# Performance work log

Measured on AMD Instinct MI355X. Metric: run time of the kernel, lower is better.

The kernel has to match this reference:

```python
import jax, jax.numpy as jnp
import numpy as np

B, T, N, D = 32, 12, 325, 64
H = 4           # geo_num_heads == t_num_heads
HD = D // H     # head_dim = 16
M_SP = 32       # spatial frequency modes (min(32, N//2))
M_T = T // 2    # temporal frequency modes (all low modes)
SCALE = HD ** -0.5


def _lin(x, W):
    # torch nn.Linear (no bias): y = x @ W.T, W: [out, in]
    return jnp.einsum('btnd,ed->btne', x, W)


def _spatial(x, Wq, Wk, Wv, weights_Q, sp_modes):
    # FEDformer-style frequency attention over the node axis N
    q, k, v = _lin(x, Wq), _lin(x, Wk), _lin(x, Wv)          # [B,T,N,D]
    prep = lambda y: y.reshape(B, T, N, H, HD).transpose(0, 1, 3, 4, 2)  # [B,T,H,HD,N]
    qn = prep(q) / jnp.linalg.norm(q)   # global Frobenius norm (torch.norm with no dim)
    kn = prep(k) / jnp.linalg.norm(k)
    vn = prep(v)
    # rfft over nodes, gather selected modes (scatter-into-zeros in torch == gather here
    # since target indices are 0..M-1)
    qf = jnp.fft.rfft(qn, axis=-1)[..., sp_modes]            # [B,T,H,HD,M] c64
    kf = jnp.fft.rfft(kn, axis=-1)[..., sp_modes]
    vf = jnp.fft.rfft(vn, axis=-1)[..., sp_modes]
    M = M_SP
    qg = qf.transpose(0, 1, 2, 4, 3)[:, :, :, :, None, :]    # [B,T,H,M,1,HD]
    wq = jnp.broadcast_to(weights_Q.astype(jnp.complex64), (B, T, H, M, M - 1, HD))
    q_cat = jnp.concatenate([qg, wq], axis=4)                # [B,T,H,M,M,HD]
    kg = kf.transpose(0, 1, 2, 4, 3)[:, :, :, None, :, :]    # [B,T,H,1,M,HD]
    att = kg * jnp.conj(q_cat) * SCALE                       # [B,T,H,M,M,HD] c64
    att = jax.nn.softmax(jnp.abs(att), axis=-2).astype(jnp.complex64)
    att = att.transpose(0, 1, 2, 3, 5, 4)                    # [B,T,H,M,HD,M]
    vg = vf[:, :, :, None, :, :]                             # [B,T,H,1,HD,M]
    out = (vg * jnp.conj(att)).mean(axis=3)                  # [B,T,H,HD,M]
    out_ft = jnp.zeros((B, T, H, HD, N // 2 + 1), jnp.complex64).at[..., sp_modes].set(out)
    y = jnp.fft.irfft(out_ft, n=N, axis=-1)                  # [B,T,H,HD,N]
    return y.transpose(0, 1, 4, 2, 3).reshape(B, T, N, D)


def _temporal(x, Wq, Wk, Wv, weights_Q_t, t_modes):
    # frequency attention over the time axis T with causal (tril) mask.
    # NOTE: torch reshapes the [B,T,N,D] buffer directly as [B,N,T,H,HD] (raw view),
    # so we replicate that exact buffer reinterpretation.
    q, k, v = _lin(x, Wq), _lin(x, Wk), _lin(x, Wv)
    prep = lambda y: y.reshape(B, N, T, H, HD).transpose(0, 1, 3, 4, 2)  # [B,N,H,HD,T]
    qn = prep(q); kn = prep(k); vn = prep(v)
    qn = qn / jnp.linalg.norm(qn)
    kn = kn / jnp.linalg.norm(kn)
    qf = jnp.fft.rfft(qn, axis=-1)[..., t_modes]             # [B,N,H,HD,Mt]
    kf = jnp.fft.rfft(kn, axis=-1)[..., t_modes]
    vf = jnp.fft.rfft(vn, axis=-1)[..., t_modes]
    Mt = M_T
    qg = qf.transpose(0, 1, 2, 4, 3)[:, :, :, :, None, :]    # [B,N,H,Mt,1,HD]
    wq = jnp.broadcast_to(weights_Q_t.astype(jnp.complex64), (B, N, H, Mt, Mt - 1, HD))
    q_cat = jnp.concatenate([qg, wq], axis=4)                # [B,N,H,Mt,Mt,HD]
    kg = kf.transpose(0, 1, 2, 4, 3)[:, :, :, :, None, :]    # [B,N,H,Mt,1,HD] (unsqueeze(4) in torch)
    att = kg * jnp.conj(q_cat) * SCALE                       # [B,N,H,Mt,Mt,HD]
    att = att.transpose(0, 1, 2, 5, 3, 4)                    # [B,N,H,HD,Mt,Mt]
    mask = jnp.tril(jnp.ones((Mt, Mt), jnp.float32))
    att = att * mask                                         # zero above diagonal
    attw = jax.nn.softmax(jnp.abs(att), axis=-1).astype(jnp.complex64)
    vg = vf[..., None]                                       # [B,N,H,HD,Mt,1]
    out = (vg * jnp.conj(attw)).mean(axis=-1)                # [B,N,H,HD,Mt]
    out_ft = jnp.zeros((B, N, H, HD, T // 2 + 1), jnp.complex64).at[..., t_modes].set(out)
    y = jnp.fft.irfft(out_ft, n=T, axis=-1)                  # [B,N,H,HD,T]
    return y.transpose(0, 4, 1, 2, 3).reshape(B, T, N, D)


def _gcn(x, adj, W_fc1, W_mlp, b_mlp):
    a = adj / jnp.sum(adj, axis=1, keepdims=True)            # row-normalized
    agg = jnp.einsum('btkd,nk->btnd', x, a)
    h = jnp.einsum('btnd,ed->btne', agg, W_fc1)              # fc1 (no bias)
    return jnp.einsum('btnd,ed->btne', h, W_mlp) + b_mlp     # mlp (bias)


def _forward(x, adj, Wq_geo, Wk_geo, Wv_geo, Wq_t, Wk_t, Wv_t,
             W_fc1, W_mlp, b_mlp, weights_Q, weights_Q_t, sp_modes, t_modes):
    gcn_out = _gcn(x, adj, W_fc1, W_mlp, b_mlp)
    sp_x = _spatial(x, Wq_geo, Wk_geo, Wv_geo, weights_Q, sp_modes)
    te_x = _temporal(x, Wq_t, Wk_t, Wv_t, weights_Q_t, t_modes)
    return gcn_out + sp_x + te_x   # proj_drop is identity (p=0)


def setup_inputs() -> dict:
    key = jax.random.key(0)
    ks = jax.random.split(key, 13)
    w = lambda k, s: jax.random.normal(k, s, dtype=jnp.float32) * 0.05
    rng = np.random.default_rng(0)
    sp_modes = np.sort(rng.permutation(N // 2)[:M_SP]).astype(np.int32)
    t_modes = np.arange(M_T, dtype=np.int32)  # modes_T == T//2 selects all low modes
    return {
        'x': jax.random.normal(ks[0], (B, T, N, D), dtype=jnp.float32),
        'adj': jax.random.uniform(ks[1], (N, N), dtype=jnp.float32),
        'Wq_geo': w(ks[2], (D, D)), 'Wk_geo': w(ks[3], (D, D)), 'Wv_geo': w(ks[4], (D, D)),
        'Wq_t': w(ks[5], (D, D)), 'Wk_t': w(ks[6], (D, D)), 'Wv_t': w(ks[7], (D, D)),
        'W_fc1': w(ks[8], (D, D)), 'W_mlp': w(ks[9], (D, D)), 'b_mlp': w(ks[10], (D,)),
        'weights_Q': jax.random.normal(ks[11], (M_SP, M_SP - 1, HD), dtype=jnp.float32),
        'weights_Q_t': jax.random.normal(ks[12], (M_T, M_T - 1, HD), dtype=jnp.float32),
        'sp_modes': jnp.asarray(sp_modes),
        't_modes': jnp.asarray(t_modes),
    }


def reference(x, adj, Wq_geo, Wk_geo, Wv_geo, Wq_t, Wk_t, Wv_t,
              W_fc1, W_mlp, b_mlp, weights_Q, weights_Q_t, sp_modes, t_modes):
    return _forward(x, adj, Wq_geo, Wk_geo, Wv_geo, Wq_t, Wk_t, Wv_t,
                    W_fc1, W_mlp, b_mlp, weights_Q, weights_Q_t, sp_modes, t_modes)
```

## Files before the change

kernel.cpp:

```cpp
#include <hip/hip_runtime.h>


typedef unsigned short u16;
typedef short short8 __attribute__((ext_vector_type(8)));
typedef float floatx4 __attribute__((ext_vector_type(4)));

__device__ __forceinline__ u16 f2bf(float f) {
  union { float fp; unsigned int u; } v; v.fp = f;
  unsigned int x = v.u;
  x += 0x7FFF + ((x >> 16) & 1);
  return (u16)(x >> 16);
}

constexpr size_t OFF_NORM = 4096;
constexpr size_t OFF_WQA  = 8208;
constexpr size_t OFF_ANB  = 24080;
constexpr size_t OFF_TB   = 81280;
constexpr size_t OFF_T2   = 102080;
constexpr size_t OFF_XCT  = 898912;
constexpr size_t OFF_WBB  = 5224288;
constexpr size_t OFF_WSPB = 5230432;
constexpr size_t OFF_WVTB = 5236576;
constexpr size_t OFF_SQQ  = 5240000;
constexpr size_t OFF_SQK  = 6026432;
constexpr size_t OFF_VFR  = 6812864;
constexpr size_t OFF_VFI  = 7599296;
constexpr size_t OFF_XA   = 13211488;

__global__ __launch_bounds__(256) void k_prep(const float* __restrict__ Wmlp,
                                              const float* __restrict__ Wfc1,
                                              const float* __restrict__ wQ,
                                              const float* __restrict__ Wq,
                                              const float* __restrict__ Wk,
                                              const float* __restrict__ Wv,
                                              const int* __restrict__ sp_modes,
                                              float* __restrict__ ws) {
  const int tid = threadIdx.x;
  const int blk = blockIdx.x;
  u16* WBBu = (u16*)(ws + OFF_WBB);
  if (blk == 0) {
    for (int i = tid; i < 512; i += 256) ws[OFF_NORM + i] = 0.f;
    for (int o = tid; o < 4096; o += 256) {
      int g = o >> 6, dd = o & 63;
      float s = 0.f;
      for (int e = 0; e < 64; ++e)
        s = fmaf(Wmlp[g * 64 + e], Wfc1[e * 64 + dd], s);
      WBBu[o] = f2bf(s);
    }
  } else if (blk < 9) {
    for (int i = (blk - 1) * 256 + tid; i < 15872; i += 2048)
      ws[OFF_WQA + i] = fabsf(wQ[i]);
  } else if (blk < 21) {
    const int j = blk - 9;
    u16* T2B = (u16*)(ws + OFF_T2);
    u16* TB = (u16*)(ws + OFF_TB);
    for (int jj = j; jj < 32; jj += 12) {
      const int f = sp_modes[jj];
      const float wgt = (f == 0) ? 1.f : 2.f;
      const int row_re = 8 * (jj >> 2) + (jj & 3);
      const int row_im = row_re + 4;
      for (int n = tid; n < 352; n += 256) {
        float c = 0.f, s = 0.f;
        if (n < 325) {
          int mm = (f * n) % 325;
          float th = 6.283185307179586f * (float)mm * (1.f / 325.f);
          c = cosf(th);
          s = sinf(th);
        }
        TB[(size_t)row_re * 352 + n] = f2bf(c);
        TB[(size_t)row_im * 352 + n] = f2bf(-s);
        if (n < 325) {
          T2B[(size_t)n * 64 + 2 * jj] = f2bf(wgt * (1.f / 325.f) * c);
          T2B[(size_t)n * 64 + 2 * jj + 1] = f2bf(-wgt * (1.f / 325.f) * s);
        }
      }
    }
  } else if (blk == 21) {
    u16* WSPBu = (u16*)(ws + OFF_WSPB);
    for (int i = tid; i < 12288; i += 256) {
      const int r = i >> 6, e = i & 63;
      const float* src = (r < 64) ? Wq : (r < 128) ? Wk : Wv;
      WSPBu[i] = f2bf(src[(size_t)(r & 63) * 64 + e]);
    }
  } else {
    for (int i = tid; i < 8192; i += 256) {
      const int r = i >> 6, e = i & 63;
      const float* src = (r < 64) ? Wq : Wk;
      WBBu[4096 + i] = f2bf(src[(size_t)(r & 63) * 64 + e]);
    }
  }
}

__global__ __launch_bounds__(256) void k_mega(const float* __restrict__ x,
                                              const float* __restrict__ adj,
                                              const float* __restrict__ Wvt,
                                              float* __restrict__ ws) {
  __shared__ __align__(16) float smem[11520];
  const int tid = threadIdx.x;
  const int blk = blockIdx.x;
  const int lane = tid & 63, wv = tid >> 6;
  const int lc = lane & 15, quad = lane >> 4;

  if (blk < 384) {
    const int bt = blk;
    u16* XBu = (u16*)smem;

    const u16* TB = (const u16*)(ws + OFF_TB);
    const u16* WSPBu = (const u16*)(ws + OFF_WSPB);
    const float* xb = x + (size_t)bt * 20800;
    const int br = tid & 31, be0 = (tid >> 5) * 8;

    {
      float va[4][8];
#pragma unroll
      for (int g = 0; g < 3; ++g) {
        const int nkc = (g < 2) ? 4 : 3;
#pragma unroll
        for (int u = 0; u < 4; ++u) {
          if (u >= nkc) break;
          const int k0 = (g * 4 + u) * 32;
          if (k0 + br < 325) {
            const float* src = xb + (size_t)(k0 + br) * 64 + be0;
            *(float4*)&va[u][0] = *(const float4*)src;
            *(float4*)&va[u][4] = *(const float4*)(src + 4);
          } else {
#pragma unroll
            for (int w = 0; w < 8; ++w) va[u][w] = 0.f;
          }
        }
#pragma unroll
        for (int u = 0; u < 4; ++u) {
          if (u >= nkc) break;
          const int k0 = (g * 4 + u) * 32;
#pragma unroll
          for (int w = 0; w < 8; ++w)
            XBu[(be0 + w) * 360 + k0 + br] = f2bf(va[u][w]);
        }
      }
    }
    __syncthreads();

    floatx4 accA[4] = {};
#pragma unroll
    for (int kc = 0; kc < 11; ++kc) {
      const short8 af = *(const short8*)&TB[(size_t)(16 * wv + lc) * 352 + kc * 32 + quad * 8];
#pragma unroll
      for (int t = 0; t < 4; ++t) {
        const short8 bf_ = *(const short8*)&XBu[(t * 16 + lc) * 360 + kc * 32 + quad * 8];
        accA[t] = __builtin_amdgcn_mfma_f32_16x16x32_bf16(af, bf_, accA[t], 0, 0, 0);
      }
    }
    __syncthreads();

    u16* xfl2 = XBu;
#pragma unroll
    for (int t = 0; t < 4; ++t)
#pragma unroll
      for (int r = 0; r < 4; ++r)
        xfl2[(t >> 1) * 2560 + (16 * wv + quad * 4 + r) * 40 + (t & 1) * 16 + lc] =
            f2bf(accA[t][r]);
    __syncthreads();

    floatx4 acc2[12] = {};
#pragma unroll
    for (int kc2 = 0; kc2 < 2; ++kc2) {
      const short8 af2 = *(const short8*)&xfl2[kc2 * 2560 + (16 * wv + lc) * 40 + quad * 8];
#pragma unroll
      for (int t = 0; t < 12; ++t) {
        const short8 bf2 = *(const short8*)&WSPBu[(t * 16 + lc) * 64 + kc2 * 32 + quad * 8];
        acc2[t] = __builtin_amdgcn_mfma_f32_16x16x32_bf16(af2, bf2, acc2[t], 0, 0, 0);
      }
    }

    float* g_sqq = ws + OFF_SQQ + (size_t)bt * 2048;
    float* g_sqk = ws + OFF_SQK + (size_t)bt * 2048;
    float* g_vfr = ws + OFF_VFR + (size_t)bt * 2048;
    float* g_vfi = ws + OFF_VFI + (size_t)bt * 2048;
    {
      const int fb = 8 * wv + ((quad >= 2) ? 4 : 0);
      const int isim = quad & 1;
#pragma unroll
      for (int t = 0; t < 12; ++t) {
        const int mat = t >> 2;
        const int d = (t & 3) * 16 + lc;
#pragma unroll
        for (int r = 0; r < 4; ++r) {
          const float v = acc2[t][r];
          if (mat == 2) {
            if (isim) g_vfi[(fb + r) * 64 + d] = v;
            else g_vfr[(fb + r) * 64 + d] = v;
          } else {
            const float s2 = v * v + __shfl_xor(v * v, 16);
            if (!isim) {
              if (mat == 0) g_sqq[(fb + r) * 64 + d] = sqrtf(s2);
              else g_sqk[(fb + r) * 64 + d] = sqrtf(s2);
            }
          }
        }
      }
    }
  } else if (blk < 1359) {
    const int blk2 = blk - 384;
    u16* XAu = (u16*)smem;
    float* red = smem + 4608;
    const size_t base = (size_t)blk2 * 128;
    const u16* WBBu = (const u16*)(ws + OFF_WBB);

    for (int i = tid; i < 2048; i += 256) {
      const int row = i >> 4, e0 = (i & 15) * 4;
      const float4 v = *(const float4*)(x + (base + row) * 64 + e0);
      u16* dst = &XAu[row * 72 + e0];
      dst[0] = f2bf(v.x); dst[1] = f2bf(v.y); dst[2] = f2bf(v.z); dst[3] = f2bf(v.w);
    }
    __syncthreads();

    short8 afc[2][2];
#pragma unroll
    for (int kc = 0; kc < 2; ++kc)
#pragma unroll
      for (int mi = 0; mi < 2; ++mi)
        afc[mi][kc] = *(const short8*)&XAu[(32 * wv + 16 * mi + lc) * 72 + kc * 32 + quad * 8];

    floatx4 acc[2][4] = {};
#pragma unroll
    for (int kc = 0; kc < 2; ++kc)
#pragma unroll
      for (int ni = 0; ni < 4; ++ni) {
        const short8 bf_ = *(const short8*)&WBBu[(ni * 16 + lc) * 64 + kc * 32 + quad * 8];
#pragma unroll
        for (int mi = 0; mi < 2; ++mi)
          acc[mi][ni] = __builtin_amdgcn_mfma_f32_16x16x32_bf16(afc[mi][kc], bf_, acc[mi][ni], 0, 0, 0);
      }

    float sq = 0.f, sk = 0.f;
#pragma unroll
    for (int ni = 0; ni < 8; ++ni) {
      floatx4 a0 = {}, a1 = {};
#pragma unroll
      for (int kc = 0; kc < 2; ++kc) {
        const short8 bf_ = *(const short8*)&WBBu[
            (size_t)(64 + (ni >> 2) * 64 + (ni & 3) * 16 + lc) * 64 + kc * 32 + quad * 8];
        a0 = __builtin_amdgcn_mfma_f32_16x16x32_bf16(afc[0][kc], bf_, a0, 0, 0, 0);
        a1 = __builtin_amdgcn_mfma_f32_16x16x32_bf16(afc[1][kc], bf_, a1, 0, 0, 0);
      }
      float s = 0.f;
#pragma unroll
      for (int reg = 0; reg < 4; ++reg)
        s = fmaf(a0[reg], a0[reg], fmaf(a1[reg], a1[reg], s));
      if (ni < 4) sq += s; else sk += s;
    }
    for (int off = 32; off > 0; off >>= 1) {
      sq += __shfl_down(sq, off);
      sk += __shfl_down(sk, off);
    }
    if (lane == 0) { red[wv] = sq; red[8 + wv] = sk; }
    __syncthreads();

    u16* xcT = XAu;
#pragma unroll
    for (int ni = 0; ni < 4; ++ni)
#pragma unroll
      for (int mi = 0; mi < 2; ++mi)
#pragma unroll
        for (int reg = 0; reg < 4; ++reg)
          xcT[(ni * 16 + lc) * 132 + 32 * wv + 16 * mi + quad * 4 + reg] =
              f2bf(acc[mi][ni][reg]);
    __syncthreads();
    u16* XCT = (u16*)(ws + OFF_XCT);
    for (int i = tid; i < 8192; i += 256) {
      const int d = i >> 7, r = i & 127;
      const unsigned int row = (unsigned int)(base + r);
      const unsigned int bt = row / 325u;
      const unsigned int n = row - bt * 325u;
      XCT[(size_t)bt * 22528 + (size_t)d * 352 + n] = xcT[d * 132 + r];
    }
    if (tid == 0)
      atomicAdd(&ws[OFF_NORM + 32 * (size_t)(blk2 & 15) + 0],
                red[0] + red[1] + red[2] + red[3]);
    if (tid == 1)
      atomicAdd(&ws[OFF_NORM + 32 * (size_t)(blk2 & 15) + 1],
                red[8] + red[9] + red[10] + red[11]);
  } else if (blk < 2009) {
    const int idx = (blk - 1359) * 256 + tid;
    if (idx >= 32 * 325 * 16) return;
    const int dq = idx & 15;
    const int n = (idx >> 4) % 325;
    const int b = idx / (16 * 325);
    const float* xp = x + ((size_t)b * 3900 + (size_t)n * 12) * 64 + dq * 4;
    float4 s = make_float4(0.f, 0.f, 0.f, 0.f);
    float sign = 1.f;
    for (int k = 0; k < 12; ++k) {
      const float4 v = *(const float4*)(xp + (size_t)k * 64);
      s.x += sign * v.x; s.y += sign * v.y; s.z += sign * v.z; s.w += sign * v.w;
      sign = -sign;
    }
    *(float4*)(ws + OFF_XA + ((size_t)b * 325 + n) * 64 + dq * 4) = s;
  } else if (blk < 2334) {
    const int n = blk - 2009;
    float* red = smem;
    float p = 0.f;
    for (int k = tid; k < 325; k += 256) p += adj[n * 325 + k];
    red[tid] = p;
    __syncthreads();
    for (int s2 = 128; s2 > 0; s2 >>= 1) {
      if (tid < s2) red[tid] += red[tid + s2];
      __syncthreads();
    }
    const float inv = 1.f / red[0];
    u16* ANB = (u16*)(ws + OFF_ANB);
    for (int k = tid; k < 352; k += 256)
      ANB[(size_t)n * 352 + k] = (k < 325) ? f2bf(adj[n * 325 + k] * inv) : (u16)0;
  } else if (blk < 2430) {
    const int idx = (blk - 2334) * 256 + tid;
    u16* p = (u16*)(ws + OFF_XCT) + (size_t)(idx >> 6) * 22528 + (size_t)(idx & 63) * 352;
    for (int c = 325; c < 352; ++c) p[c] = 0;
  } else {
    u16* WVTBu = (u16*)(ws + OFF_WVTB);
    for (int i = tid; i < 4096; i += 256) WVTBu[i] = f2bf(Wvt[i]);
  }
}

__global__ __launch_bounds__(256) void k_final3(const float* __restrict__ x,
                                                const float* __restrict__ bmlp,
                                                float* __restrict__ ws,
                                                float* __restrict__ out) {
  __shared__ __align__(16) float smem[8448];
  float* asq = smem;
  float* askl = smem + 2048;
  float* wbar = smem + 4096;
  unsigned int* oftu = (unsigned int*)(smem + 6144);
  const u16* oft16 = (const u16*)oftu;

  const int tid = threadIdx.x;
  const int bt = blockIdx.x / 3, mc = blockIdx.x % 3;
  const int m0 = mc * 128;
  const int wave = tid >> 6, lane = tid & 63;
  const int quad = lane >> 4, lc = lane & 15;

  float nq = 0.f, nk = 0.f;
#pragma unroll
  for (int k2 = 0; k2 < 16; ++k2) {
    const float2 v = *(const float2*)(ws + OFF_NORM + 32 * (size_t)k2);
    nq += v.x; nk += v.y;
  }
  const float inv_nq = rsqrtf(nq);
  const float inv_nk = rsqrtf(nk);

  for (int i = tid; i < 2048; i += 256) {
    asq[i] = ws[OFF_SQQ + (size_t)bt * 2048 + i];
    askl[i] = 0.25f * inv_nk * ws[OFF_SQK + (size_t)bt * 2048 + i];
    wbar[i] = 0.f;
  }
  __syncthreads();
  {
    const int d = tid & 63, fb2 = tid >> 6, hd = d & 15;
    const float* wqa = ws + OFF_WQA;
    float wacc[32];
#pragma unroll
    for (int j = 0; j < 32; ++j) wacc[j] = 0.f;
    for (int r8 = 0; r8 < 8; ++r8) {
      const int m = fb2 + (r8 << 2);
      const float aq = inv_nq * asq[m * 64 + d];
      float sv[32];
      float mx = -1e30f;
#pragma unroll
      for (int j = 0; j < 32; ++j) {
        const float a = (j == 0) ? aq : wqa[(m * 31 + (j - 1)) * 16 + hd];
        const float s = askl[j * 64 + d] * a;
        sv[j] = s;
        mx = fmaxf(mx, s);
      }
      float sum = 0.f;
#pragma unroll
      for (int j = 0; j < 32; ++j) {
        const float ev = __expf(sv[j] - mx);
        sv[j] = ev;
        sum += ev;
      }
      const float sc = 0.03125f / sum;
#pragma unroll
      for (int j = 0; j < 32; ++j) wacc[j] += sv[j] * sc;
    }
#pragma unroll
    for (int j = 0; j < 32; ++j) atomicAdd(&wbar[j * 64 + d], wacc[j]);
  }
  __syncthreads();
  for (int i2 = tid; i2 < 2048; i2 += 256) {
    const int j = i2 >> 6, d = i2 & 63;
    const float w = wbar[j * 64 + d];
    const unsigned int lo = f2bf(ws[OFF_VFR + (size_t)bt * 2048 + j * 64 + d] * w);
    const unsigned int hi = f2bf(ws[OFF_VFI + (size_t)bt * 2048 + j * 64 + d] * w);
    oftu[d * 36 + j] = lo | (hi << 16);
  }
  __syncthreads();

  const u16* ANB = (const u16*)(ws + OFF_ANB);
  const u16* T2B = (const u16*)(ws + OFF_T2);
  const u16* XCT = (const u16*)(ws + OFF_XCT) + (size_t)bt * 22528;
  const u16* WVTBu = (const u16*)(ws + OFF_WVTB);

  const int b = bt / 12, t = bt - b * 12;
  const float sgn12 = ((t & 1) ? -1.f : 1.f) * (1.f / 12.f);

  floatx4 acc[2][4] = {};

#pragma unroll
  for (int c13 = 0; c13 < 13; ++c13) {
    const bool gcn = (c13 < 11);
    const int acol = gcn ? c13 * 32 : (c13 - 11) * 32;
    short8 af[2], bf_[4];
#pragma unroll
    for (int mi = 0; mi < 2; ++mi) {
      const int gr = m0 + wave * 32 + mi * 16 + lc;
      short8 a = {};
      if (gr < 325)
        a = gcn ? *(const short8*)&ANB[(size_t)gr * 352 + acol + quad * 8]
                : *(const short8*)&T2B[(size_t)gr * 64 + acol + quad * 8];
      af[mi] = a;
    }
#pragma unroll
    for (int ni = 0; ni < 4; ++ni)
      bf_[ni] = gcn ? *(const short8*)&XCT[(size_t)(ni * 16 + lc) * 352 + acol + quad * 8]
                    : *(const short8*)&oft16[(ni * 16 + lc) * 72 + acol + quad * 8];
#pragma unroll
    for (int mi = 0; mi < 2; ++mi)
#pragma unroll
      for (int ni = 0; ni < 4; ++ni)
        acc[mi][ni] = __builtin_amdgcn_mfma_f32_16x16x32_bf16(
            af[mi], bf_[ni], acc[mi][ni], 0, 0, 0);
  }

#pragma unroll
  for (int kc = 0; kc < 2; ++kc) {
    const int k0 = kc * 32 + quad * 8;
    short8 af[2];
#pragma unroll
    for (int mi = 0; mi < 2; ++mi) {
      const int nr = m0 + wave * 32 + mi * 16 + lc;
      short8 a = {};
      if (nr < 325) {
        const float* xp = x + ((size_t)b * 3900 + (size_t)nr * 12 + t) * 64 + k0;
        const float* xap = ws + OFF_XA + ((size_t)b * 325 + nr) * 64 + k0;
        float xv[8], av[8];
        *(float4*)xv = *(const float4*)xp;
        *(float4*)(xv + 4) = *(const float4*)(xp + 4);
        *(float4*)av = *(const float4*)xap;
        *(float4*)(av + 4) = *(const float4*)(xap + 4);
#pragma unroll
        for (int u = 0; u < 8; ++u)
          a[u] = (short)f2bf((xv[u] - sgn12 * av[u]) * (1.f / 6.f));
      }
      af[mi] = a;
    }
#pragma unroll
    for (int ni = 0; ni < 4; ++ni) {
      const short8 bf_ = *(const short8*)&WVTBu[(size_t)(ni * 16 + lc) * 64 + k0];
#pragma unroll
      for (int mi = 0; mi < 2; ++mi)
        acc[mi][ni] = __builtin_amdgcn_mfma_f32_16x16x32_bf16(
            af[mi], bf_, acc[mi][ni], 0, 0, 0);
    }
  }

#pragma unroll
  for (int ni = 0; ni < 4; ++ni) {
    const int d = ni * 16 + lc;
    const float bias = bmlp[d];
#pragma unroll
    for (int mi = 0; mi < 2; ++mi) {
#pragma unroll
      for (int reg = 0; reg < 4; ++reg) {
        const int n = m0 + wave * 32 + mi * 16 + quad * 4 + reg;
        if (n >= 325) continue;
        out[((size_t)bt * 325 + n) * 64 + d] = acc[mi][ni][reg] + bias;
      }
    }
  }
}

extern "C" void kernel_launch(void* const* d_in, const int* in_sizes, int n_in,
                              void* d_out, int out_size, void* d_ws, size_t ws_size,
                              hipStream_t stream) {
  const float* x = (const float*)d_in[0];
  const float* adj = (const float*)d_in[1];
  const float* Wq_g = (const float*)d_in[2];
  const float* Wk_g = (const float*)d_in[3];
  const float* Wv_g = (const float*)d_in[4];
  const float* Wv_t = (const float*)d_in[7];
  const float* Wfc1 = (const float*)d_in[8];
  const float* Wmlp = (const float*)d_in[9];
  const float* bmlp = (const float*)d_in[10];
  const float* wQ = (const float*)d_in[11];
  const int* sp_modes = (const int*)d_in[13];
  float* ws = (float*)d_ws;
  float* out = (float*)d_out;

  (void)in_sizes; (void)n_in; (void)out_size; (void)ws_size;

  k_prep<<<23, 256, 0, stream>>>(Wmlp, Wfc1, wQ, Wq_g, Wk_g, Wv_g, sp_modes, ws);
  k_mega<<<2431, 256, 0, stream>>>(x, adj, Wv_t, ws);
  k_final3<<<1152, 256, 0, stream>>>(x, bmlp, ws, out);
}
```

Measured before the change: 281.1 us.

## Hoist per-bt spectral softmax into separate kernel, swizzle final block order

```diff
diff --git a/kernel.cpp b/kernel.cpp
--- a/kernel.cpp
+++ b/kernel.cpp
@@ -17,6 +17,7 @@
 constexpr size_t OFF_ANB  = 24080;
 constexpr size_t OFF_TB   = 81280;
 constexpr size_t OFF_T2   = 102080;
+constexpr size_t OFF_OFT  = 112480;
 constexpr size_t OFF_XCT  = 898912;
 constexpr size_t OFF_WBB  = 5224288;
 constexpr size_t OFF_WSPB = 5230432;
@@ -92,8 +93,6 @@
 }
 
 __global__ __launch_bounds__(256) void k_mega(const float* __restrict__ x,
-                                              const float* __restrict__ adj,
-                                              const float* __restrict__ Wvt,
                                               float* __restrict__ ws) {
   __shared__ __align__(16) float smem[11520];
   const int tid = threadIdx.x;
@@ -280,7 +279,7 @@
     if (tid == 1)
       atomicAdd(&ws[OFF_NORM + 32 * (size_t)(blk2 & 15) + 1],
                 red[8] + red[9] + red[10] + red[11]);
-  } else if (blk < 2009) {
+  } else {
     const int idx = (blk - 1359) * 256 + tid;
     if (idx >= 32 * 325 * 16) return;
     const int dq = idx & 15;
@@ -295,8 +294,84 @@
       sign = -sign;
     }
     *(float4*)(ws + OFF_XA + ((size_t)b * 325 + n) * 64 + dq * 4) = s;
-  } else if (blk < 2334) {
-    const int n = blk - 2009;
+  }
+}
+
+__global__ __launch_bounds__(256) void k_phasec(const float* __restrict__ adj,
+                                                const float* __restrict__ Wvt,
+                                                float* __restrict__ ws) {
+  __shared__ __align__(16) float smem[10240];
+  const int tid = threadIdx.x;
+  const int blk = blockIdx.x;
+
+  if (blk < 384) {
+    const int bt = blk;
+    float* asq = smem;
+    float* askl = smem + 2048;
+    float* vfre = smem + 4096;
+    float* vfim = smem + 6144;
+    float* wbar = smem + 8192;
+
+    float g_nq = 0.f, g_nk = 0.f;
+#pragma unroll
+    for (int k2 = 0; k2 < 16; ++k2) {
+      const float2 v = *(const float2*)(ws + OFF_NORM + 32 * (size_t)k2);
+      g_nq += v.x; g_nk += v.y;
+    }
+    const float inv_nq = rsqrtf(g_nq);
+    const float inv_nk = rsqrtf(g_nk);
+
+    for (int i = tid; i < 2048; i += 256) {
+      asq[i] = ws[OFF_SQQ + (size_t)bt * 2048 + i];
+      askl[i] = 0.25f * inv_nk * ws[OFF_SQK + (size_t)bt * 2048 + i];
+      vfre[i] = ws[OFF_VFR + (size_t)bt * 2048 + i];
+      vfim[i] = ws[OFF_VFI + (size_t)bt * 2048 + i];
+      wbar[i] = 0.f;
+    }
+    __syncthreads();
+    {
+      const int d = tid & 63, fb2 = tid >> 6, hd = d & 15;
+      const float* wqa = ws + OFF_WQA;
+      float wacc[32];
+#pragma unroll
+      for (int j = 0; j < 32; ++j) wacc[j] = 0.f;
+      for (int r8 = 0; r8 < 8; ++r8) {
+        const int m = fb2 + (r8 << 2);
+        const float aq = inv_nq * asq[m * 64 + d];
+        float sv[32];
+        float mx = -1e30f;
+#pragma unroll
+        for (int j = 0; j < 32; ++j) {
+          const float a = (j == 0) ? aq : wqa[(m * 31 + (j - 1)) * 16 + hd];
+          const float s = askl[j * 64 + d] * a;
+          sv[j] = s;
+          mx = fmaxf(mx, s);
+        }
+        float sum = 0.f;
+#pragma unroll
+        for (int j = 0; j < 32; ++j) {
+          const float ev = __expf(sv[j] - mx);
+          sv[j] = ev;
+          sum += ev;
+        }
+        const float sc = 0.03125f / sum;
+#pragma unroll
+        for (int j = 0; j < 32; ++j) wacc[j] += sv[j] * sc;
+      }
+#pragma unroll
+      for (int j = 0; j < 32; ++j) atomicAdd(&wbar[j * 64 + d], wacc[j]);
+    }
+    __syncthreads();
+    unsigned int* OFTu = (unsigned int*)(ws + OFF_OFT) + (size_t)bt * 2048;
+    for (int i2 = tid; i2 < 2048; i2 += 256) {
+      const int d = i2 >> 5, j = i2 & 31;
+      const float w = wbar[j * 64 + d];
+      const unsigned int lo = f2bf(vfre[j * 64 + d] * w);
+      const unsigned int hi = f2bf(vfim[j * 64 + d] * w);
+      OFTu[i2] = lo | (hi << 16);
+    }
+  } else if (blk < 709) {
+    const int n = blk - 384;
     float* red = smem;
     float p = 0.f;
     for (int k = tid; k < 325; k += 256) p += adj[n * 325 + k];
@@ -310,8 +385,8 @@
     u16* ANB = (u16*)(ws + OFF_ANB);
     for (int k = tid; k < 352; k += 256)
       ANB[(size_t)n * 352 + k] = (k < 325) ? f2bf(adj[n * 325 + k] * inv) : (u16)0;
-  } else if (blk < 2430) {
-    const int idx = (blk - 2334) * 256 + tid;
+  } else if (blk < 805) {
+    const int idx = (blk - 709) * 256 + tid;
     u16* p = (u16*)(ws + OFF_XCT) + (size_t)(idx >> 6) * 22528 + (size_t)(idx & 63) * 352;
     for (int c = 325; c < 352; ++c) p[c] = 0;
   } else {
@@ -320,83 +395,21 @@
   }
 }
 
-__global__ __launch_bounds__(256) void k_final3(const float* __restrict__ x,
+__global__ __launch_bounds__(256) void k_final2(const float* __restrict__ x,
                                                 const float* __restrict__ bmlp,
                                                 float* __restrict__ ws,
                                                 float* __restrict__ out) {
-  __shared__ __align__(16) float smem[8448];
-  float* asq = smem;
-  float* askl = smem + 2048;
-  float* wbar = smem + 4096;
-  unsigned int* oftu = (unsigned int*)(smem + 6144);
-  const u16* oft16 = (const u16*)oftu;
-
   const int tid = threadIdx.x;
-  const int bt = blockIdx.x / 3, mc = blockIdx.x % 3;
+  const int wg = (blockIdx.x & 7) * 144 + (blockIdx.x >> 3);
+  const int bt = wg / 3, mc = wg % 3;
   const int m0 = mc * 128;
   const int wave = tid >> 6, lane = tid & 63;
   const int quad = lane >> 4, lc = lane & 15;
 
-  float nq = 0.f, nk = 0.f;
-#pragma unroll
-  for (int k2 = 0; k2 < 16; ++k2) {
-    const float2 v = *(const float2*)(ws + OFF_NORM + 32 * (size_t)k2);
-    nq += v.x; nk += v.y;
-  }
-  const float inv_nq = rsqrtf(nq);
-  const float inv_nk = rsqrtf(nk);
-
-  for (int i = tid; i < 2048; i += 256) {
-    asq[i] = ws[OFF_SQQ + (size_t)bt * 2048 + i];
-    askl[i] = 0.25f * inv_nk * ws[OFF_SQK + (size_t)bt * 2048 + i];
-    wbar[i] = 0.f;
-  }
-  __syncthreads();
-  {
-    const int d = tid & 63, fb2 = tid >> 6, hd = d & 15;
-    const float* wqa = ws + OFF_WQA;
-    float wacc[32];
-#pragma unroll
-    for (int j = 0; j < 32; ++j) wacc[j] = 0.f;
-    for (int r8 = 0; r8 < 8; ++r8) {
-      const int m = fb2 + (r8 << 2);
-      const float aq = inv_nq * asq[m * 64 + d];
-      float sv[32];
-      float mx = -1e30f;
-#pragma unroll
-      for (int j = 0; j < 32; ++j) {
-        const float a = (j == 0) ? aq : wqa[(m * 31 + (j - 1)) * 16 + hd];
-        const float s = askl[j * 64 + d] * a;
-        sv[j] = s;
-        mx = fmaxf(mx, s);
-      }
-      float sum = 0.f;
-#pragma unroll
-      for (int j = 0; j < 32; ++j) {
-        const float ev = __expf(sv[j] - mx);
-        sv[j] = ev;
-        sum += ev;
-      }
-      const float sc = 0.03125f / sum;
-#pragma unroll
-      for (int j = 0; j < 32; ++j) wacc[j] += sv[j] * sc;
-    }
-#pragma unroll
-    for (int j = 0; j < 32; ++j) atomicAdd(&wbar[j * 64 + d], wacc[j]);
-  }
-  __syncthreads();
-  for (int i2 = tid; i2 < 2048; i2 += 256) {
-    const int j = i2 >> 6, d = i2 & 63;
-    const float w = wbar[j * 64 + d];
-    const unsigned int lo = f2bf(ws[OFF_VFR + (size_t)bt * 2048 + j * 64 + d] * w);
-    const unsigned int hi = f2bf(ws[OFF_VFI + (size_t)bt * 2048 + j * 64 + d] * w);
-    oftu[d * 36 + j] = lo | (hi << 16);
-  }
-  __syncthreads();
-
   const u16* ANB = (const u16*)(ws + OFF_ANB);
   const u16* T2B = (const u16*)(ws + OFF_T2);
   const u16* XCT = (const u16*)(ws + OFF_XCT) + (size_t)bt * 22528;
+  const u16* OFT = (const u16*)(ws + OFF_OFT) + (size_t)bt * 4096;
   const u16* WVTBu = (const u16*)(ws + OFF_WVTB);
 
   const int b = bt / 12, t = bt - b * 12;
@@ -407,21 +420,23 @@
 #pragma unroll
   for (int c13 = 0; c13 < 13; ++c13) {
     const bool gcn = (c13 < 11);
+    const u16* Asrc = gcn ? ANB : T2B;
+    const int astr = gcn ? 352 : 64;
     const int acol = gcn ? c13 * 32 : (c13 - 11) * 32;
+    const u16* Bsrc = gcn ? XCT : OFT;
+    const int bstr = gcn ? 352 : 64;
     short8 af[2], bf_[4];
 #pragma unroll
     for (int mi = 0; mi < 2; ++mi) {
       const int gr = m0 + wave * 32 + mi * 16 + lc;
       short8 a = {};
       if (gr < 325)
-        a = gcn ? *(const short8*)&ANB[(size_t)gr * 352 + acol + quad * 8]
-                : *(const short8*)&T2B[(size_t)gr * 64 + acol + quad * 8];
+        a = *(const short8*)&Asrc[(size_t)gr * astr + acol + quad * 8];
       af[mi] = a;
     }
 #pragma unroll
     for (int ni = 0; ni < 4; ++ni)
-      bf_[ni] = gcn ? *(const short8*)&XCT[(size_t)(ni * 16 + lc) * 352 + acol + quad * 8]
-                    : *(const short8*)&oft16[(ni * 16 + lc) * 72 + acol + quad * 8];
+      bf_[ni] = *(const short8*)&Bsrc[(size_t)(ni * 16 + lc) * bstr + acol + quad * 8];
 #pragma unroll
     for (int mi = 0; mi < 2; ++mi)
 #pragma unroll
@@ -498,6 +513,7 @@
   (void)in_sizes; (void)n_in; (void)out_size; (void)ws_size;
 
   k_prep<<<23, 256, 0, stream>>>(Wmlp, Wfc1, wQ, Wq_g, Wk_g, Wv_g, sp_modes, ws);
-  k_mega<<<2431, 256, 0, stream>>>(x, adj, Wv_t, ws);
-  k_final3<<<1152, 256, 0, stream>>>(x, bmlp, ws, out);
+  k_mega<<<2009, 256, 0, stream>>>(x, ws);
+  k_phasec<<<806, 256, 0, stream>>>(adj, Wv_t, ws);
+  k_final2<<<1152, 256, 0, stream>>>(x, bmlp, ws, out);
 }
```

New measurement: 237.1 us. 15.6% less time.

## Process all node chunks per block to avoid recomputing spectral softmax weights

Applied to the files above, without the earlier changes.

```diff
diff --git a/kernel.cpp b/kernel.cpp
--- a/kernel.cpp
+++ b/kernel.cpp
@@ -320,35 +320,38 @@
   }
 }
 
-__global__ __launch_bounds__(256) void k_final3(const float* __restrict__ x,
+__global__ __launch_bounds__(256) void k_final4(const float* __restrict__ x,
                                                 const float* __restrict__ bmlp,
                                                 float* __restrict__ ws,
                                                 float* __restrict__ out) {
-  __shared__ __align__(16) float smem[8448];
+  __shared__ __align__(16) float smem[10240];
   float* asq = smem;
   float* askl = smem + 2048;
-  float* wbar = smem + 4096;
-  unsigned int* oftu = (unsigned int*)(smem + 6144);
+  float* vfre = smem + 4096;
+  float* vfim = smem + 6144;
+  float* wbar = smem + 8192;
+  unsigned int* oftu = (unsigned int*)smem;
   const u16* oft16 = (const u16*)oftu;
 
   const int tid = threadIdx.x;
-  const int bt = blockIdx.x / 3, mc = blockIdx.x % 3;
-  const int m0 = mc * 128;
+  const int bt = blockIdx.x;
   const int wave = tid >> 6, lane = tid & 63;
   const int quad = lane >> 4, lc = lane & 15;
 
-  float nq = 0.f, nk = 0.f;
+  float g_nq = 0.f, g_nk = 0.f;
 #pragma unroll
   for (int k2 = 0; k2 < 16; ++k2) {
     const float2 v = *(const float2*)(ws + OFF_NORM + 32 * (size_t)k2);
-    nq += v.x; nk += v.y;
-  }
-  const float inv_nq = rsqrtf(nq);
-  const float inv_nk = rsqrtf(nk);
+    g_nq += v.x; g_nk += v.y;
+  }
+  const float inv_nq = rsqrtf(g_nq);
+  const float inv_nk = rsqrtf(g_nk);
 
   for (int i = tid; i < 2048; i += 256) {
     asq[i] = ws[OFF_SQQ + (size_t)bt * 2048 + i];
     askl[i] = 0.25f * inv_nk * ws[OFF_SQK + (size_t)bt * 2048 + i];
+    vfre[i] = ws[OFF_VFR + (size_t)bt * 2048 + i];
+    vfim[i] = ws[OFF_VFI + (size_t)bt * 2048 + i];
     wbar[i] = 0.f;
   }
   __syncthreads();
@@ -388,8 +391,8 @@
   for (int i2 = tid; i2 < 2048; i2 += 256) {
     const int j = i2 >> 6, d = i2 & 63;
     const float w = wbar[j * 64 + d];
-    const unsigned int lo = f2bf(ws[OFF_VFR + (size_t)bt * 2048 + j * 64 + d] * w);
-    const unsigned int hi = f2bf(ws[OFF_VFI + (size_t)bt * 2048 + j * 64 + d] * w);
+    const unsigned int lo = f2bf(vfre[j * 64 + d] * w);
+    const unsigned int hi = f2bf(vfim[j * 64 + d] * w);
     oftu[d * 36 + j] = lo | (hi << 16);
   }
   __syncthreads();
@@ -402,80 +405,91 @@
   const int b = bt / 12, t = bt - b * 12;
   const float sgn12 = ((t & 1) ? -1.f : 1.f) * (1.f / 12.f);
 
-  floatx4 acc[2][4] = {};
+  floatx4 acc[3][2][4] = {};
 
 #pragma unroll
   for (int c13 = 0; c13 < 13; ++c13) {
     const bool gcn = (c13 < 11);
     const int acol = gcn ? c13 * 32 : (c13 - 11) * 32;
-    short8 af[2], bf_[4];
-#pragma unroll
-    for (int mi = 0; mi < 2; ++mi) {
-      const int gr = m0 + wave * 32 + mi * 16 + lc;
-      short8 a = {};
-      if (gr < 325)
-        a = gcn ? *(const short8*)&ANB[(size_t)gr * 352 + acol + quad * 8]
-                : *(const short8*)&T2B[(size_t)gr * 64 + acol + quad * 8];
-      af[mi] = a;
-    }
+    short8 bf_[4];
 #pragma unroll
     for (int ni = 0; ni < 4; ++ni)
       bf_[ni] = gcn ? *(const short8*)&XCT[(size_t)(ni * 16 + lc) * 352 + acol + quad * 8]
                     : *(const short8*)&oft16[(ni * 16 + lc) * 72 + acol + quad * 8];
 #pragma unroll
-    for (int mi = 0; mi < 2; ++mi)
-#pragma unroll
-      for (int ni = 0; ni < 4; ++ni)
-        acc[mi][ni] = __builtin_amdgcn_mfma_f32_16x16x32_bf16(
-            af[mi], bf_[ni], acc[mi][ni], 0, 0, 0);
+    for (int mc = 0; mc < 3; ++mc) {
+      short8 af[2];
+#pragma unroll
+      for (int mi = 0; mi < 2; ++mi) {
+        const int gr = mc * 128 + wave * 32 + mi * 16 + lc;
+        short8 a = {};
+        if (gr < 325)
+          a = gcn ? *(const short8*)&ANB[(size_t)gr * 352 + acol + quad * 8]
+                  : *(const short8*)&T2B[(size_t)gr * 64 + acol + quad * 8];
+        af[mi] = a;
+      }
+#pragma unroll
+      for (int mi = 0; mi < 2; ++mi)
+#pragma unroll
+        for (int ni = 0; ni < 4; ++ni)
+          acc[mc][mi][ni] = __builtin_amdgcn_mfma_f32_16x16x32_bf16(
+              af[mi], bf_[ni], acc[mc][mi][ni], 0, 0, 0);
+    }
   }
 
 #pragma unroll
   for (int kc = 0; kc < 2; ++kc) {
     const int k0 = kc * 32 + quad * 8;
-    short8 af[2];
-#pragma unroll
-    for (int mi = 0; mi < 2; ++mi) {
-      const int nr = m0 + wave * 32 + mi * 16 + lc;
-      short8 a = {};
-      if (nr < 325) {
-        const float* xp = x + ((size_t)b * 3900 + (size_t)nr * 12 + t) * 64 + k0;
-        const float* xap = ws + OFF_XA + ((size_t)b * 325 + nr) * 64 + k0;
-        float xv[8], av[8];
-        *(float4*)xv = *(const float4*)xp;
-        *(float4*)(xv + 4) = *(const float4*)(xp + 4);
-        *(float4*)av = *(const float4*)xap;
-        *(float4*)(av + 4) = *(const float4*)(xap + 4);
-#pragma unroll
-        for (int u = 0; u < 8; ++u)
-          a[u] = (short)f2bf((xv[u] - sgn12 * av[u]) * (1.f / 6.f));
-      }
-      af[mi] = a;
-    }
+    short8 bf_[4];
+#pragma unroll
+    for (int ni = 0; ni < 4; ++ni)
+      bf_[ni] = *(const short8*)&WVTBu[(size_t)(ni * 16 + lc) * 64 + k0];
+#pragma unroll
+    for (int mc = 0; mc < 3; ++mc) {
+      short8 af[2];
+#pragma unroll
+      for (int mi = 0; mi < 2; ++mi) {
+        const int nr = mc * 128 + wave * 32 + mi * 16 + lc;
+        short8 a = {};
+        if (nr < 325) {
+          const float* xp = x + ((size_t)b * 3900 + (size_t)nr * 12 + t) * 64 + k0;
+          const float* xap = ws + OFF_XA + ((size_t)b * 325 + nr) * 64 + k0;
+          float xv[8], av[8];
+          *(float4*)xv = *(const float4*)xp;
+          *(float4*)(xv + 4) = *(const float4*)(xp + 4);
+          *(float4*)av = *(const float4*)xap;
+          *(float4*)(av + 4) = *(const float4*)(xap + 4);
+#pragma unroll
+          for (int u = 0; u < 8; ++u)
+            a[u] = (short)f2bf((xv[u] - sgn12 * av[u]) * (1.f / 6.f));
+        }
+        af[mi] = a;
+      }
+#pragma unroll
+      for (int mi = 0; mi < 2; ++mi)
+#pragma unroll
+        for (int ni = 0; ni < 4; ++ni)
+          acc[mc][mi][ni] = __builtin_amdgcn_mfma_f32_16x16x32_bf16(
+              af[mi], bf_[ni], acc[mc][mi][ni], 0, 0, 0);
+    }
+  }
+
+#pragma unroll
+  for (int mc = 0; mc < 3; ++mc)
 #pragma unroll
     for (int ni = 0; ni < 4; ++ni) {
-      const short8 bf_ = *(const short8*)&WVTBu[(size_t)(ni * 16 + lc) * 64 + k0];
-#pragma unroll
-      for (int mi = 0; mi < 2; ++mi)
-        acc[mi][ni] = __builtin_amdgcn_mfma_f32_16x16x32_bf16(
-            af[mi], bf_, acc[mi][ni], 0, 0, 0);
-    }
-  }
-
-#pragma unroll
-  for (int ni = 0; ni < 4; ++ni) {
-    const int d = ni * 16 + lc;
-    const float bias = bmlp[d];
-#pragma unroll
-    for (int mi = 0; mi < 2; ++mi) {
-#pragma unroll
-      for (int reg = 0; reg < 4; ++reg) {
-        const int n = m0 + wave * 32 + mi * 16 + quad * 4 + reg;
-        if (n >= 325) continue;
-        out[((size_t)bt * 325 + n) * 64 + d] = acc[mi][ni][reg] + bias;
-      }
-    }
-  }
+      const int d = ni * 16 + lc;
+      const float bias = bmlp[d];
+#pragma unroll
+      for (int mi = 0; mi < 2; ++mi) {
+#pragma unroll
+        for (int reg = 0; reg < 4; ++reg) {
+          const int n = mc * 128 + wave * 32 + mi * 16 + quad * 4 + reg;
+          if (n >= 325) continue;
+          out[((size_t)bt * 325 + n) * 64 + d] = acc[mc][mi][ni][reg] + bias;
+        }
+      }
+    }
 }
 
 extern "C" void kernel_launch(void* const* d_in, const int* in_sizes, int n_in,
@@ -499,5 +513,5 @@
 
   k_prep<<<23, 256, 0, stream>>>(Wmlp, Wfc1, wQ, Wq_g, Wk_g, Wv_g, sp_modes, ws);
   k_mega<<<2431, 256, 0, stream>>>(x, adj, Wv_t, ws);
-  k_final3<<<1152, 256, 0, stream>>>(x, bmlp, ws, out);
+  k_final4<<<384, 256, 0, stream>>>(x, bmlp, ws, out);
 }
```

After: 258.3 us. 8.1% less time.
